# Kernel optimization log

Hardware: AMD Instinct MI355X
Metric: run time of the kernel (lower is better)

## Reference

```python
import jax, jax.numpy as jnp
import numpy as np

S, B, C = 7, 2, 20
D = C + 5 * B  # 30
LAMBDA_COORD = 5.0
LAMBDA_NOOBJ = 0.5
EPS = 1e-6


def _iou_yolo(b1, b2):
    # b1, b2: [..., 4] boxes in (cx, cy, w, h) 'yolo' format
    b1x1 = b1[..., 0] - b1[..., 2] / 2
    b1y1 = b1[..., 1] - b1[..., 3] / 2
    b1x2 = b1[..., 0] + b1[..., 2] / 2
    b1y2 = b1[..., 1] + b1[..., 3] / 2
    b2x1 = b2[..., 0] - b2[..., 2] / 2
    b2y1 = b2[..., 1] - b2[..., 3] / 2
    b2x2 = b2[..., 0] + b2[..., 2] / 2
    b2y2 = b2[..., 1] + b2[..., 3] / 2
    iw = jnp.clip(jnp.minimum(b1x2, b2x2) - jnp.maximum(b1x1, b2x1), 0.0)
    ih = jnp.clip(jnp.minimum(b1y2, b2y2) - jnp.maximum(b1y1, b2y1), 0.0)
    inter = iw * ih
    a1 = jnp.abs((b1x2 - b1x1) * (b1y2 - b1y1))
    a2 = jnp.abs((b2x2 - b2x1) * (b2y2 - b2y1))
    return inter / (a1 + a2 - inter + EPS)


def setup_inputs() -> dict:
    batch = 16384
    key = jax.random.key(0)
    k1, k2, k3 = jax.random.split(key, 3)
    # true coords / classes in (0.05, 0.95) so sqrt(w), sqrt(h) are well-defined
    y_trues = jax.random.uniform(k1, (batch, S, S, D), dtype=jnp.float32) * 0.9 + 0.05
    conf = (jax.random.uniform(k2, (batch, S, S)) < 0.3).astype(jnp.float32)
    y_trues = y_trues.at[..., 4].set(conf)  # objectness indicator is exactly 0 or 1
    y_preds = jax.random.normal(k3, (batch, S, S, D), dtype=jnp.float32)
    return {"y_trues": y_trues, "y_preds": y_preds}


def reference(y_trues, y_preds):
    yt = y_trues.reshape(-1, S * S, D)
    yp = y_preds.reshape(-1, S * S, D)
    batch = yt.shape[0]

    obj = (yt[..., 4] == 1.0).astype(yt.dtype)   # [N, S*S]
    noobj = 1.0 - obj

    iou1 = _iou_yolo(yt[..., 0:4], yp[..., 0:4])
    iou2 = _iou_yolo(yt[..., 0:4], yp[..., 5:9])
    best1 = iou1 > iou2                           # responsible box selection

    box_hat = jnp.where(best1[..., None], yp[..., 0:4], yp[..., 5:9])
    conf_hat = jnp.where(best1, yp[..., 4], yp[..., 9])        # responsible conf
    other_conf_hat = jnp.where(best1, yp[..., 9], yp[..., 4])  # non-responsible conf

    # xy offset loss
    xy = (yt[..., 0] - box_hat[..., 0]) ** 2 + (yt[..., 1] - box_hat[..., 1]) ** 2
    # wh loss: sqrt(true) vs sqrt(|pred + eps|)
    wh = (jnp.sqrt(yt[..., 2]) - jnp.sqrt(jnp.abs(box_hat[..., 2] + EPS))) ** 2 \
       + (jnp.sqrt(yt[..., 3]) - jnp.sqrt(jnp.abs(box_hat[..., 3] + EPS))) ** 2
    # object confidence loss (true conf == 1 in obj cells)
    obj_conf = (yt[..., 4] - conf_hat) ** 2
    # no-object penalty on the NON-responsible box inside object cells (target 0)
    noobj_in_obj = LAMBDA_NOOBJ * other_conf_hat ** 2
    # no-object penalty on BOTH boxes in cells without objects (true conf == 0)
    noobj_cells = LAMBDA_NOOBJ * ((yt[..., 4] - yp[..., 4]) ** 2
                                  + (yt[..., 4] - yp[..., 9]) ** 2)
    # class loss over C classes
    cls = jnp.sum((yt[..., 10:] - yp[..., 10:]) ** 2, axis=-1)

    per_cell = obj * (LAMBDA_COORD * (xy + wh) + obj_conf + noobj_in_obj + cls) \
             + noobj * noobj_cells
    return jnp.sum(per_cell) / batch
```

## Files before the change

### kernel.cpp

```cpp
#include <hip/hip_runtime.h>


#define SS 49
#define DD 30
#define BLOCK 256
#define CPB 256
#define TILE_F (CPB * DD)

__device__ __forceinline__ void g2l16(const float* g, float* l) {
    __builtin_amdgcn_global_load_lds(
        (const __attribute__((address_space(1))) void*)g,
        (__attribute__((address_space(3))) void*)l,
        16, 0, 0);
}

__device__ __forceinline__ float iou_yolo(const float b1[4], const float b2[4]) {
    const float EPS = 1e-6f;
    float b1x1 = b1[0] - b1[2] * 0.5f, b1y1 = b1[1] - b1[3] * 0.5f;
    float b1x2 = b1[0] + b1[2] * 0.5f, b1y2 = b1[1] + b1[3] * 0.5f;
    float b2x1 = b2[0] - b2[2] * 0.5f, b2y1 = b2[1] - b2[3] * 0.5f;
    float b2x2 = b2[0] + b2[2] * 0.5f, b2y2 = b2[1] + b2[3] * 0.5f;
    float iw = fmaxf(fminf(b1x2, b2x2) - fmaxf(b1x1, b2x1), 0.0f);
    float ih = fmaxf(fminf(b1y2, b2y2) - fmaxf(b1y1, b2y1), 0.0f);
    float inter = iw * ih;
    float a1 = fabsf((b1x2 - b1x1) * (b1y2 - b1y1));
    float a2 = fabsf((b2x2 - b2x1) * (b2y2 - b2y1));
    return inter / (a1 + a2 - inter + EPS);
}

__device__ __forceinline__ float cell_loss(const float* __restrict__ yt,
                                           const float* __restrict__ yp) {
    const float LAMBDA_COORD = 5.0f;
    const float LAMBDA_NOOBJ = 0.5f;
    const float EPS = 1e-6f;

    float obj = (yt[4] == 1.0f) ? 1.0f : 0.0f;
    float noobj = 1.0f - obj;

    float tb[4]  = {yt[0], yt[1], yt[2], yt[3]};
    float pb1[4] = {yp[0], yp[1], yp[2], yp[3]};
    float pb2[4] = {yp[5], yp[6], yp[7], yp[8]};
    float iou1 = iou_yolo(tb, pb1);
    float iou2 = iou_yolo(tb, pb2);
    bool best1 = iou1 > iou2;

    float bh0 = best1 ? yp[0] : yp[5];
    float bh1 = best1 ? yp[1] : yp[6];
    float bh2 = best1 ? yp[2] : yp[7];
    float bh3 = best1 ? yp[3] : yp[8];
    float conf_hat       = best1 ? yp[4] : yp[9];
    float other_conf_hat = best1 ? yp[9] : yp[4];

    float dx = yt[0] - bh0, dy = yt[1] - bh1;
    float xy = dx * dx + dy * dy;

    float sw = sqrtf(yt[2]) - sqrtf(fabsf(bh2 + EPS));
    float sh = sqrtf(yt[3]) - sqrtf(fabsf(bh3 + EPS));
    float wh = sw * sw + sh * sh;

    float dc = yt[4] - conf_hat;
    float obj_conf = dc * dc;

    float noobj_in_obj = LAMBDA_NOOBJ * other_conf_hat * other_conf_hat;

    float d4 = yt[4] - yp[4];
    float d9 = yt[4] - yp[9];
    float noobj_cells = LAMBDA_NOOBJ * (d4 * d4 + d9 * d9);

    float cls = 0.0f;
#pragma unroll
    for (int k = 10; k < DD; ++k) {
        float d = yt[k] - yp[k];
        cls += d * d;
    }

    return obj * (LAMBDA_COORD * (xy + wh) + obj_conf + noobj_in_obj + cls)
         + noobj * noobj_cells;
}

template <int USE_WS>
__global__ __launch_bounds__(BLOCK)
void yolo_loss_kernel(const float* __restrict__ yt_g,
                      const float* __restrict__ yp_g,
                      float* __restrict__ sink,
                      int ncells, float inv_batch) {
    __shared__ __align__(16) float lt[TILE_F];
    __shared__ __align__(16) float lp[TILE_F];

    const int tid = threadIdx.x;
    const int base_cell = blockIdx.x * CPB;
    const int nc = min(CPB, ncells - base_cell);
    const int nf = nc * DD;
    const int nf4 = nf >> 2;
    const size_t base_f = (size_t)base_cell * DD;

    const float* gt = yt_g + base_f;
    const float* gp = yp_g + base_f;

    for (int j = tid; j < nf4; j += BLOCK) {
        g2l16(gt + 4 * j, &lt[4 * j]);
        g2l16(gp + 4 * j, &lp[4 * j]);
    }
    for (int j = (nf4 << 2) + tid; j < nf; j += BLOCK) {
        lt[j] = gt[j];
        lp[j] = gp[j];
    }
    __syncthreads();

    float per_cell = 0.0f;
    if (tid < nc) per_cell = cell_loss(&lt[tid * DD], &lp[tid * DD]);

#pragma unroll
    for (int off = 32; off > 0; off >>= 1)
        per_cell += __shfl_down(per_cell, off, 64);

    __shared__ float smem[BLOCK / 64];
    int lane = threadIdx.x & 63;
    int wave = threadIdx.x >> 6;
    if (lane == 0) smem[wave] = per_cell;
    __syncthreads();
    if (threadIdx.x == 0) {
        float s = smem[0] + smem[1] + smem[2] + smem[3];
        if (USE_WS) sink[blockIdx.x] = s;
        else        atomicAdd(sink, s * inv_batch);
    }
}

__global__ __launch_bounds__(256)
void reduce_kernel(const float* __restrict__ partials, float* __restrict__ out,
                   int n, float inv_batch) {
    float s = 0.0f;
    for (int i = threadIdx.x; i < n; i += 256) s += partials[i];
#pragma unroll
    for (int off = 32; off > 0; off >>= 1)
        s += __shfl_down(s, off, 64);
    __shared__ float sm[4];
    int lane = threadIdx.x & 63;
    int wave = threadIdx.x >> 6;
    if (lane == 0) sm[wave] = s;
    __syncthreads();
    if (threadIdx.x == 0)
        out[0] = (sm[0] + sm[1] + sm[2] + sm[3]) * inv_batch;
}

extern "C" void kernel_launch(void* const* d_in, const int* in_sizes, int n_in,
                              void* d_out, int out_size, void* d_ws, size_t ws_size,
                              hipStream_t stream) {
    const float* yt = (const float*)d_in[0];
    const float* yp = (const float*)d_in[1];
    float* out = (float*)d_out;
    float* ws = (float*)d_ws;

    int total = in_sizes[0];
    int ncells = total / DD;
    int batch = ncells / SS;
    float inv_batch = 1.0f / (float)batch;

    int grid = (ncells + CPB - 1) / CPB;

    if (ws != nullptr && ws_size >= (size_t)grid * sizeof(float)) {
        yolo_loss_kernel<1><<<grid, BLOCK, 0, stream>>>(yt, yp, ws, ncells,
                                                        inv_batch);
        reduce_kernel<<<1, 256, 0, stream>>>(ws, out, grid, inv_batch);
    } else {
        hipMemsetAsync(out, 0, sizeof(float), stream);
        yolo_loss_kernel<0><<<grid, BLOCK, 0, stream>>>(yt, yp, out, ncells,
                                                        inv_batch);
    }
}
```

Baseline: 206.0 us.

## Use persistent per-wave tiles with register-staged float2 loads instead of block-wide LDS DMA

Replaces the one-tile-per-block design, which used direct global-to-LDS loads and a block barrier, with a persistent grid capped at 512 blocks. Each wave loops over its own 64-cell tiles, staging them through registers into a private LDS slice with float2 loads, so no block-wide synchronisation is needed per tile. The goal is to cut block launch and barrier overhead and keep many independent waves streaming. The cost is lower memory-level parallelism per wave, since each wave serialises its load and compute with no double buffering, and narrower 8-byte accesses.

```diff
diff --git a/kernel.cpp b/kernel.cpp
--- a/kernel.cpp
+++ b/kernel.cpp
@@ -4,15 +4,11 @@
 #define SS 49
 #define DD 30
 #define BLOCK 256
-#define CPB 256
-#define TILE_F (CPB * DD)
-
-__device__ __forceinline__ void g2l16(const float* g, float* l) {
-    __builtin_amdgcn_global_load_lds(
-        (const __attribute__((address_space(1))) void*)g,
-        (__attribute__((address_space(3))) void*)l,
-        16, 0, 0);
-}
+#define WPB 4
+#define CPW 64
+#define FPW (CPW * DD)
+#define F2PW (FPW / 2)
+#define PERSIST_GRID 512
 
 __device__ __forceinline__ float iou_yolo(const float b1[4], const float b2[4]) {
     const float EPS = 1e-6f;
@@ -84,42 +80,63 @@
                       const float* __restrict__ yp_g,
                       float* __restrict__ sink,
                       int ncells, float inv_batch) {
-    __shared__ __align__(16) float lt[TILE_F];
-    __shared__ __align__(16) float lp[TILE_F];
+    __shared__ __align__(16) float lt[WPB][FPW];
+    __shared__ __align__(16) float lp[WPB][FPW];
+    __shared__ float smem[WPB];
 
-    const int tid = threadIdx.x;
-    const int base_cell = blockIdx.x * CPB;
-    const int nc = min(CPB, ncells - base_cell);
-    const int nf = nc * DD;
-    const int nf4 = nf >> 2;
-    const size_t base_f = (size_t)base_cell * DD;
+    const int tid  = threadIdx.x;
+    const int lane = tid & 63;
+    const int wave = tid >> 6;
+    const int gwave  = blockIdx.x * WPB + wave;
+    const int nwaves = gridDim.x * WPB;
+    const int nwt = (ncells + CPW - 1) / CPW;
 
-    const float* gt = yt_g + base_f;
-    const float* gp = yp_g + base_f;
+    float* __restrict__ ltw = lt[wave];
+    float* __restrict__ lpw = lp[wave];
+    float2* __restrict__ ltw2 = reinterpret_cast<float2*>(ltw);
+    float2* __restrict__ lpw2 = reinterpret_cast<float2*>(lpw);
 
-    for (int j = tid; j < nf4; j += BLOCK) {
-        g2l16(gt + 4 * j, &lt[4 * j]);
-        g2l16(gp + 4 * j, &lp[4 * j]);
+    float wsum = 0.0f;
+
+    for (int wt = gwave; wt < nwt; wt += nwaves) {
+        const int cb = wt * CPW;
+        const size_t f2b = (size_t)cb * (DD / 2);
+        const float2* gt2 = reinterpret_cast<const float2*>(yt_g) + f2b;
+        const float2* gp2 = reinterpret_cast<const float2*>(yp_g) + f2b;
+        const int ncf2 = min(CPW, ncells - cb) * (DD / 2);
+
+        if (ncf2 == F2PW) {
+#pragma unroll
+            for (int i = 0; i < F2PW / 64; ++i) {
+                int idx = i * 64 + lane;
+                float2 a = gt2[idx];
+                float2 b = gp2[idx];
+                ltw2[idx] = a;
+                lpw2[idx] = b;
+            }
+        } else {
+#pragma unroll
+            for (int i = 0; i < F2PW / 64; ++i) {
+                int idx = i * 64 + lane;
+                if (idx < ncf2) {
+                    ltw2[idx] = gt2[idx];
+                    lpw2[idx] = gp2[idx];
+                }
+            }
+        }
+
+        int c = cb + lane;
+        if (c < ncells)
+            wsum += cell_loss(&ltw[lane * DD], &lpw[lane * DD]);
     }
-    for (int j = (nf4 << 2) + tid; j < nf; j += BLOCK) {
-        lt[j] = gt[j];
-        lp[j] = gp[j];
-    }
-    __syncthreads();
-
-    float per_cell = 0.0f;
-    if (tid < nc) per_cell = cell_loss(&lt[tid * DD], &lp[tid * DD]);
 
 #pragma unroll
     for (int off = 32; off > 0; off >>= 1)
-        per_cell += __shfl_down(per_cell, off, 64);
+        wsum += __shfl_down(wsum, off, 64);
 
-    __shared__ float smem[BLOCK / 64];
-    int lane = threadIdx.x & 63;
-    int wave = threadIdx.x >> 6;
-    if (lane == 0) smem[wave] = per_cell;
+    if (lane == 0) smem[wave] = wsum;
     __syncthreads();
-    if (threadIdx.x == 0) {
+    if (tid == 0) {
         float s = smem[0] + smem[1] + smem[2] + smem[3];
         if (USE_WS) sink[blockIdx.x] = s;
         else        atomicAdd(sink, s * inv_batch);
@@ -156,7 +173,9 @@
     int batch = ncells / SS;
     float inv_batch = 1.0f / (float)batch;
 
-    int grid = (ncells + CPB - 1) / CPB;
+    int nwt = (ncells + CPW - 1) / CPW;
+    int grid_needed = (nwt + WPB - 1) / WPB;
+    int grid = grid_needed < PERSIST_GRID ? grid_needed : PERSIST_GRID;
 
     if (ws != nullptr && ws_size >= (size_t)grid * sizeof(float)) {
         yolo_loss_kernel<1><<<grid, BLOCK, 0, stream>>>(yt, yp, ws, ncells,
```

Measured after the change: 206.7 us. Within noise of the previous version (+0.3%).
